# Kernel optimization log

Measured on AMD Instinct MI355X. Metric: run time of the kernel, lower is better.

The kernel has to match this reference:

```python
import jax, jax.numpy as jnp
import numpy as np

H = W = 128
R = 2
H2, W2 = H // R, W // R
TOPK = 3
NSEG = H * W + 1  # segment 0 = background


def _ccl(binary):
    """8-connected component labeling via iterative max-label propagation.
    binary: [H,W] bool. Returns int32 labels, 0 = background; each component
    gets a unique (arbitrary) positive id = max pixel index in the component."""
    idx = jnp.arange(1, H * W + 1, dtype=jnp.int32).reshape(H, W)
    lab0 = jnp.where(binary, idx, 0)

    def cond(c):
        return c[1]

    def body(c):
        lab, _ = c
        nb = jax.lax.reduce_window(lab, jnp.int32(0), jax.lax.max,
                                   (3, 3), (1, 1), 'SAME')  # 3x3 incl. self
        new = jnp.where(binary, nb, 0)
        return new, jnp.any(new != lab)

    lab, _ = jax.lax.while_loop(cond, body, (lab0, jnp.bool_(True)))
    return lab


def _process_one(prob_i, feat_i):
    """prob_i: [1,H,W], feat_i: [Cf,H,W] -> [3*Cf, H2, W2]."""
    p = prob_i[0]
    binary = p > 0.5
    lab = _ccl(binary).reshape(-1)  # [H*W] segment ids

    ones = jnp.ones((H * W,), jnp.float32)
    count = jax.ops.segment_sum(ones, lab, num_segments=NSEG)
    conf_sum = jax.ops.segment_sum(p.reshape(-1), lab, num_segments=NSEG)
    mean_conf = conf_sum / jnp.maximum(count, 1.0)

    rows = jnp.repeat(jnp.arange(H, dtype=jnp.int32), W)
    cols = jnp.tile(jnp.arange(W, dtype=jnp.int32), H)
    min_r = jax.ops.segment_min(rows, lab, num_segments=NSEG)
    max_r = jax.ops.segment_max(rows, lab, num_segments=NSEG)
    min_c = jax.ops.segment_min(cols, lab, num_segments=NSEG)
    max_c = jax.ops.segment_max(cols, lab, num_segments=NSEG)

    valid = (count > 0) & (jnp.arange(NSEG) > 0)
    score = jnp.where(valid, mean_conf, -jnp.inf)
    _, top_idx = jax.lax.top_k(score, TOPK)  # regions sorted by mean confidence
    K = jnp.sum(valid.astype(jnp.int32))     # number of connected regions

    # duplication rules: K==0 -> full image x3; K==1 -> [f0,f0,f0];
    # K==2 -> [f0,f0,f1]; K>=3 -> [f0,f1,f2]
    i0, i1 = top_idx[0], top_idx[1]
    slots = jnp.where(K >= 3, top_idx,
            jnp.where(K == 2, jnp.stack([i0, i0, i1]),
                      jnp.stack([i0, i0, i0])))

    mr = jnp.where(K > 0, min_r[slots], 0)
    Mr = jnp.where(K > 0, max_r[slots] + 1, H)  # bbox half-open, regionprops style
    mc = jnp.where(K > 0, min_c[slots], 0)
    Mc = jnp.where(K > 0, max_c[slots] + 1, W)

    def crop(a, b, c, d):
        # PyTorch nearest interpolate: src = floor(dst * in/out)
        r = a + (jnp.arange(H2) * (b - a)) // H2
        cc = c + (jnp.arange(W2) * (d - c)) // W2
        return feat_i[:, r][:, :, cc]  # [Cf, H2, W2]

    out = jax.vmap(crop)(mr, Mr, mc, Mc)  # [3, Cf, H2, W2]
    return out.reshape(-1, H2, W2)         # [3*Cf, H2, W2]


def setup_inputs() -> dict:
    key = jax.random.key(0)
    k1, k2 = jax.random.split(key)
    prob = jax.random.uniform(k1, (16, 1, H, W), dtype=jnp.float32)
    feat = jax.random.normal(k2, (16, 192, H, W), dtype=jnp.float32)
    return {"prob": prob, "feat": feat}


def reference(prob, feat):
    return jax.vmap(_process_one)(prob, feat)  # [B, 3*Cf, H2, W2]
```

## Files before the change

### kernel.cpp

```cpp
#include <hip/hip_runtime.h>
#include <limits.h>

#define HH 128
#define WW_ 128
#define HW 16384
#define NB 16
#define CF 192
#define H2 64
#define W2 64
#define NRUN 8192
#define NCOMP 4096

typedef float vf4 __attribute__((ext_vector_type(4)));
typedef unsigned long long ull;


__device__ inline int uf_find(int* par, int x) {
    volatile int* vp = (volatile int*)par;
    int p = vp[x];
    while (p != x) {
        int g = vp[p];
        vp[x] = g;
        x = g;
        p = vp[x];
    }
    return x;
}

__device__ inline void uf_union(int* par, int a, int b) {
    int ra = uf_find(par, a);
    int rb = uf_find(par, b);
    while (ra != rb) {
        if (ra < rb) { int t = ra; ra = rb; rb = t; }
        int old = atomicCAS(&par[ra], ra, rb);
        if (old == ra) return;
        ra = uf_find(par, old);
        rb = uf_find(par, rb);
    }
}


__device__ inline int getbit2(ull lo, ull hi, int c) {
    return (int)(((c < 64) ? (lo >> c) : (hi >> (c - 64))) & 1ULL);
}

__device__ inline int leading_ones(ull v) {
    ull nv = ~v;
    return (nv == 0ULL) ? 64 : __clzll(nv);
}

__device__ inline int trailing_ones(ull v) {
    ull nv = ~v;
    return (nv == 0ULL) ? 64 : (__ffsll(nv) - 1);
}

__device__ inline int run_start_col(ull lo, ull hi, int c) {
    if (c < 64) {
        int ones = leading_ones(lo << (63 - c));
        return c - ones + 1;
    }
    int ones = leading_ones(hi << (127 - c));
    int rs = c - ones + 1;
    if (rs == 64) rs -= leading_ones(lo);
    return rs;
}

__device__ inline int run_end_col(ull lo, ull hi, int c) {
    if (c >= 64) {
        return c + trailing_ones(hi >> (c - 64)) - 1;
    }
    int e = c + trailing_ones(lo >> c) - 1;
    if (e == 63) e += trailing_ones(hi);
    return e;
}

__device__ inline int run_index(ull rs_lo, ull rs_hi, int cs) {
    if (cs < 64)  return __popcll(rs_lo & ((1ULL << cs) - 1ULL));
    if (cs == 64) return __popcll(rs_lo);
    return __popcll(rs_lo) + __popcll(rs_hi & ((1ULL << (cs - 64)) - 1ULL));
}

__device__ inline void top3_ins(float s, int id, int x,
    float& s0, float& s1, float& s2,
    int& i0, int& i1, int& i2,
    int& x0, int& x1, int& x2)
{
    if (x < 0) return;
    if (s > s0 || (s == s0 && id < i0)) {
        s2 = s1; i2 = i1; x2 = x1;
        s1 = s0; i1 = i0; x1 = x0;
        s0 = s;  i0 = id; x0 = x;
    } else if (s > s1 || (s == s1 && id < i1)) {
        s2 = s1; i2 = i1; x2 = x1;
        s1 = s;  i1 = id; x1 = x;
    } else if (s > s2 || (s == s2 && id < i2)) {
        s2 = s;  i2 = id; x2 = x;
    }
}


__global__ __launch_bounds__(1024) void ccl_kernel(
    const float* __restrict__ prob, int* __restrict__ bbox)
{
    __shared__ int parent[NRUN];
    __shared__ ull rowmask[HH][2];
    __shared__ ull rsmask[HH][2];
    __shared__ int nrunrow[HH];
    __shared__ int   lcnt[NCOMP];
    __shared__ float lconf[NCOMP];
    __shared__ int lminr[NCOMP], lmaxr[NCOMP];
    __shared__ int lminc[NCOMP], lmaxc[NCOMP];
    __shared__ int lmaxid[NCOMP];
    __shared__ int snroots;
    __shared__ float wss[48];
    __shared__ int wid_[48], wrx[48];

    const int b = blockIdx.x;
    const int tid = threadIdx.x;
    const float* p = prob + (size_t)b * HW;

    if (tid == 0) snroots = 0;

    #pragma unroll
    for (int k = 0; k < HW / 1024; ++k) {
        int i = k * 1024 + tid;
        ull m = __ballot(p[i] > 0.5f);
        if ((tid & 63) == 0) rowmask[i >> 7][(i >> 6) & 1] = m;
    }
    for (int j = tid; j < NCOMP; j += 1024) {
        lcnt[j] = 0; lconf[j] = 0.f;
        lminr[j] = INT_MAX; lmaxr[j] = -1;
        lminc[j] = INT_MAX; lmaxc[j] = -1;
        lmaxid[j] = 0;
    }
    __syncthreads();

    for (int r = tid; r < HH; r += 1024) {
        ull lo = rowmask[r][0], hi = rowmask[r][1];
        ull rs_lo = lo & ~(lo << 1);
        ull rs_hi = hi & ~((hi << 1) | (lo >> 63));
        rsmask[r][0] = rs_lo; rsmask[r][1] = rs_hi;
        nrunrow[r] = __popcll(rs_lo) + __popcll(rs_hi);
    }
    __syncthreads();

    for (int rid = tid; rid < NRUN; rid += 1024)
        if ((rid & 63) < nrunrow[rid >> 6]) parent[rid] = rid;
    __syncthreads();

    for (int s = 1; s <= 64; s <<= 1) {
        const int items = (64 / s) * WW_;
        for (int it = tid; it < items; it += 1024) {
            int k = it >> 7, c = it & 127;
            int r = s * (2 * k + 1);
            ull lo = rowmask[r][0], hi = rowmask[r][1];
            if (!getbit2(lo, hi, c)) continue;
            ull ulo = rowmask[r - 1][0], uhi = rowmask[r - 1][1];
            int l  = (c > 0)   ? getbit2(lo, hi, c - 1) : 0;
            int rt = (c < 127) ? getbit2(lo, hi, c + 1) : 0;
            int up = getbit2(ulo, uhi, c);
            int ul = (c > 0)   ? getbit2(ulo, uhi, c - 1) : 0;
            int ur = (c < 127) ? getbit2(ulo, uhi, c + 1) : 0;
            bool u1 = up && !(l && ul);
            bool u2 = !up && ul && !l;
            bool u3 = !up && ur && !rt;
            if (!(u1 | u2 | u3)) continue;
            ull rs_lo = rsmask[r][0], rs_hi = rsmask[r][1];
            ull urs_lo = rsmask[r - 1][0], urs_hi = rsmask[r - 1][1];
            int rid = (r << 6) + run_index(rs_lo, rs_hi, run_start_col(lo, hi, c));
            int ub = (r - 1) << 6;
            if (u1) uf_union(parent, rid, ub + run_index(urs_lo, urs_hi, run_start_col(ulo, uhi, c)));
            if (u2) uf_union(parent, rid, ub + run_index(urs_lo, urs_hi, run_start_col(ulo, uhi, c - 1)));
            if (u3) uf_union(parent, rid, ub + run_index(urs_lo, urs_hi, run_start_col(ulo, uhi, c + 1)));
        }
        __syncthreads();
        for (int rid = tid; rid < NRUN; rid += 1024)
            if ((rid & 63) < nrunrow[rid >> 6]) parent[rid] = uf_find(parent, rid);
        __syncthreads();
    }

    for (int rid = tid; rid < NRUN; rid += 1024) {
        if ((rid & 63) < nrunrow[rid >> 6] && parent[rid] == rid) {
            int idx = atomicAdd(&snroots, 1);
            parent[rid] = NRUN + idx;
        }
    }
    __syncthreads();

    {
        int row = tid >> 3;
        int w0 = (tid & 7) * 16;
        ull lo = rowmask[row][0], hi = rowmask[row][1];
        ull rs_lo = rsmask[row][0], rs_hi = rsmask[row][1];
        ull seg = ((w0 < 64) ? (rs_lo >> w0) : (rs_hi >> (w0 - 64))) & 0xFFFFULL;
        int curIdx = -1, aCnt = 0, aMinc = 0, aMaxc = 0, aMaxid = 0;
        float aConf = 0.f;
        while (seg) {
            int c = w0 + (__ffsll(seg) - 1);
            seg &= seg - 1;
            int e = run_end_col(lo, hi, c);
            int rid = (row << 6) + run_index(rs_lo, rs_hi, c);
            int v = parent[rid];
            int idx = (v >= NRUN) ? (v - NRUN) : (parent[v] - NRUN);
            float s = 0.f;
            for (int j = c; j <= e; ++j) s += p[(row << 7) + j];
            if (idx == curIdx) {
                aCnt += e - c + 1; aConf += s;
                aMaxc = e; aMaxid = (row << 7) + e + 1;
            } else {
                if (curIdx >= 0) {
                    atomicAdd(&lcnt[curIdx], aCnt);
                    atomicAdd(&lconf[curIdx], aConf);
                    atomicMin(&lminr[curIdx], row);
                    atomicMax(&lmaxr[curIdx], row);
                    atomicMin(&lminc[curIdx], aMinc);
                    atomicMax(&lmaxc[curIdx], aMaxc);
                    atomicMax(&lmaxid[curIdx], aMaxid);
                }
                curIdx = idx; aCnt = e - c + 1; aConf = s;
                aMinc = c; aMaxc = e; aMaxid = (row << 7) + e + 1;
            }
        }
        if (curIdx >= 0) {
            atomicAdd(&lcnt[curIdx], aCnt);
            atomicAdd(&lconf[curIdx], aConf);
            atomicMin(&lminr[curIdx], row);
            atomicMax(&lmaxr[curIdx], row);
            atomicMin(&lminc[curIdx], aMinc);
            atomicMax(&lmaxc[curIdx], aMaxc);
            atomicMax(&lmaxid[curIdx], aMaxid);
        }
    }
    __syncthreads();

    const int n = snroots;
    float s0 = -INFINITY, s1 = -INFINITY, s2 = -INFINITY;
    int i0 = INT_MAX, i1 = INT_MAX, i2 = INT_MAX;
    int x0 = -1, x1 = -1, x2 = -1;
    for (int j = tid; j < n; j += 1024) {
        float s = lconf[j] / (float)lcnt[j];
        top3_ins(s, lmaxid[j], j, s0, s1, s2, i0, i1, i2, x0, x1, x2);
    }
    for (int off = 32; off; off >>= 1) {
        float bs0 = __shfl_xor(s0, off), bs1 = __shfl_xor(s1, off), bs2 = __shfl_xor(s2, off);
        int bi0 = __shfl_xor(i0, off), bi1 = __shfl_xor(i1, off), bi2 = __shfl_xor(i2, off);
        int bx0 = __shfl_xor(x0, off), bx1 = __shfl_xor(x1, off), bx2 = __shfl_xor(x2, off);
        top3_ins(bs0, bi0, bx0, s0, s1, s2, i0, i1, i2, x0, x1, x2);
        top3_ins(bs1, bi1, bx1, s0, s1, s2, i0, i1, i2, x0, x1, x2);
        top3_ins(bs2, bi2, bx2, s0, s1, s2, i0, i1, i2, x0, x1, x2);
    }
    if ((tid & 63) == 0) {
        int w = tid >> 6;
        wss[w * 3 + 0] = s0; wid_[w * 3 + 0] = i0; wrx[w * 3 + 0] = x0;
        wss[w * 3 + 1] = s1; wid_[w * 3 + 1] = i1; wrx[w * 3 + 1] = x1;
        wss[w * 3 + 2] = s2; wid_[w * 3 + 2] = i2; wrx[w * 3 + 2] = x2;
    }
    __syncthreads();

    if (tid == 0) {
        float t0 = -INFINITY, t1 = -INFINITY, t2 = -INFINITY;
        int ti0 = INT_MAX, ti1 = INT_MAX, ti2 = INT_MAX;
        int tx0 = -1, tx1 = -1, tx2 = -1;
        for (int t = 0; t < 48; ++t)
            top3_ins(wss[t], wid_[t], wrx[t], t0, t1, t2, ti0, ti1, ti2, tx0, tx1, tx2);
        int K = n;
        int roots[3];
        if (K >= 3)      { roots[0] = tx0; roots[1] = tx1; roots[2] = tx2; }
        else if (K == 2) { roots[0] = tx0; roots[1] = tx0; roots[2] = tx1; }
        else             { roots[0] = tx0; roots[1] = tx0; roots[2] = tx0; }
        for (int slot = 0; slot < 3; ++slot) {
            int mr, h, mc, w;
            if (K == 0) { mr = 0; h = HH; mc = 0; w = WW_; }
            else {
                int rt = roots[slot];
                mr = lminr[rt]; h = lmaxr[rt] + 1 - mr;
                mc = lminc[rt]; w = lmaxc[rt] + 1 - mc;
            }
            int* o = bbox + (b * 3 + slot) * 4;
            o[0] = mr; o[1] = h; o[2] = mc; o[3] = w;
        }
    }
}


__global__ __launch_bounds__(256) void crop_kernel(
    const float* __restrict__ feat, const int* __restrict__ bbox,
    float* __restrict__ out)
{
    const int gid = blockIdx.x * 256 + threadIdx.x;
    const int x4 = gid & 15;
    const int y  = (gid >> 4) & 63;
    const int t  = gid >> 10;
    const int c  = t % CF;
    const int bs = t / CF;
    const int* bb = bbox + bs * 4;
    const int mr = bb[0], h = bb[1], mc = bb[2], w = bb[3];
    const int r = mr + ((y * h) >> 6);
    const int bimg = bs / 3;
    const float* row = feat + (((size_t)bimg * CF + c) * HH + r) * WW_;
    const int x = x4 * 4;
    vf4 v;
    v.x = row[mc + (((x + 0) * w) >> 6)];
    v.y = row[mc + (((x + 1) * w) >> 6)];
    v.z = row[mc + (((x + 2) * w) >> 6)];
    v.w = row[mc + (((x + 3) * w) >> 6)];
    __builtin_nontemporal_store(v, (vf4*)out + gid);
}


extern "C" void kernel_launch(void* const* d_in, const int* in_sizes, int n_in,
                              void* d_out, int out_size, void* d_ws, size_t ws_size,
                              hipStream_t stream) {
    const float* prob = (const float*)d_in[0];
    const float* feat = (const float*)d_in[1];
    float* out = (float*)d_out;

    int* bbox = (int*)d_ws;

    hipLaunchKernelGGL(ccl_kernel, dim3(NB), dim3(1024), 0, stream,
                       prob, bbox);
    const int total4 = NB * 3 * CF * H2 * (W2 / 4);
    hipLaunchKernelGGL(crop_kernel, dim3(total4 / 256), dim3(256), 0, stream,
                       feat, bbox, out);
}
```

Before: 399.9 us.

## Single-pass union-find CCL, stage probabilities in LDS, bbox only for winners

Drops the hierarchical log-step merge schedule, which ran 7 rounds of unions each followed by a full path-compression pass, and replaces it with one pass of concurrent unions over all rows and then a single compression. Probability values are cached in shared memory so per-run confidence sums no longer reread global memory. Root numbering uses a wave ballot with one atomic per wave instead of one atomic per root. Bounding boxes are computed in a second scan only for the three winning components, which removes four per-component atomic arrays and the run-merging logic. In exchange, run-level atomics now fire per run instead of per merged segment, and heavy concurrent unions may contend more.

```diff
diff --git a/kernel.cpp b/kernel.cpp
--- a/kernel.cpp
+++ b/kernel.cpp
@@ -103,17 +103,18 @@
     const float* __restrict__ prob, int* __restrict__ bbox)
 {
     __shared__ int parent[NRUN];
+    __shared__ float pbuf[HW];
     __shared__ ull rowmask[HH][2];
     __shared__ ull rsmask[HH][2];
     __shared__ int nrunrow[HH];
     __shared__ int   lcnt[NCOMP];
     __shared__ float lconf[NCOMP];
-    __shared__ int lminr[NCOMP], lmaxr[NCOMP];
-    __shared__ int lminc[NCOMP], lmaxc[NCOMP];
     __shared__ int lmaxid[NCOMP];
     __shared__ int snroots;
     __shared__ float wss[48];
     __shared__ int wid_[48], wrx[48];
+    __shared__ int winner[3];
+    __shared__ int w_minr[3], w_maxr[3], w_minc[3], w_maxc[3];
 
     const int b = blockIdx.x;
     const int tid = threadIdx.x;
@@ -124,14 +125,15 @@
     #pragma unroll
     for (int k = 0; k < HW / 1024; ++k) {
         int i = k * 1024 + tid;
-        ull m = __ballot(p[i] > 0.5f);
+        float v = p[i];
+        pbuf[i] = v;
+        ull m = __ballot(v > 0.5f);
         if ((tid & 63) == 0) rowmask[i >> 7][(i >> 6) & 1] = m;
     }
+    #pragma unroll
+    for (int k = 0; k < NRUN / 1024; ++k) parent[k * 1024 + tid] = k * 1024 + tid;
     for (int j = tid; j < NCOMP; j += 1024) {
-        lcnt[j] = 0; lconf[j] = 0.f;
-        lminr[j] = INT_MAX; lmaxr[j] = -1;
-        lminc[j] = INT_MAX; lmaxc[j] = -1;
-        lmaxid[j] = 0;
+        lcnt[j] = 0; lconf[j] = 0.f; lmaxid[j] = 0;
     }
     __syncthreads();
 
@@ -144,46 +146,46 @@
     }
     __syncthreads();
 
+    for (int k = 0; k < HW / 1024; ++k) {
+        int i = k * 1024 + tid;
+        int r = i >> 7, c = i & 127;
+        if (r == 0) continue;
+        ull lo = rowmask[r][0], hi = rowmask[r][1];
+        if (!getbit2(lo, hi, c)) continue;
+        ull ulo = rowmask[r - 1][0], uhi = rowmask[r - 1][1];
+        int l  = (c > 0)   ? getbit2(lo, hi, c - 1) : 0;
+        int rt = (c < 127) ? getbit2(lo, hi, c + 1) : 0;
+        int up = getbit2(ulo, uhi, c);
+        int ul = (c > 0)   ? getbit2(ulo, uhi, c - 1) : 0;
+        int ur = (c < 127) ? getbit2(ulo, uhi, c + 1) : 0;
+        bool u1 = up && !(l && ul);
+        bool u2 = !up && ul && !l;
+        bool u3 = !up && ur && !rt;
+        if (!(u1 | u2 | u3)) continue;
+        ull rs_lo = rsmask[r][0], rs_hi = rsmask[r][1];
+        ull urs_lo = rsmask[r - 1][0], urs_hi = rsmask[r - 1][1];
+        int rid = (r << 6) + run_index(rs_lo, rs_hi, run_start_col(lo, hi, c));
+        int ub = (r - 1) << 6;
+        if (u1) uf_union(parent, rid, ub + run_index(urs_lo, urs_hi, run_start_col(ulo, uhi, c)));
+        if (u2) uf_union(parent, rid, ub + run_index(urs_lo, urs_hi, run_start_col(ulo, uhi, c - 1)));
+        if (u3) uf_union(parent, rid, ub + run_index(urs_lo, urs_hi, run_start_col(ulo, uhi, c + 1)));
+    }
+    __syncthreads();
+
     for (int rid = tid; rid < NRUN; rid += 1024)
-        if ((rid & 63) < nrunrow[rid >> 6]) parent[rid] = rid;
-    __syncthreads();
-
-    for (int s = 1; s <= 64; s <<= 1) {
-        const int items = (64 / s) * WW_;
-        for (int it = tid; it < items; it += 1024) {
-            int k = it >> 7, c = it & 127;
-            int r = s * (2 * k + 1);
-            ull lo = rowmask[r][0], hi = rowmask[r][1];
-            if (!getbit2(lo, hi, c)) continue;
-            ull ulo = rowmask[r - 1][0], uhi = rowmask[r - 1][1];
-            int l  = (c > 0)   ? getbit2(lo, hi, c - 1) : 0;
-            int rt = (c < 127) ? getbit2(lo, hi, c + 1) : 0;
-            int up = getbit2(ulo, uhi, c);
-            int ul = (c > 0)   ? getbit2(ulo, uhi, c - 1) : 0;
-            int ur = (c < 127) ? getbit2(ulo, uhi, c + 1) : 0;
-            bool u1 = up && !(l && ul);
-            bool u2 = !up && ul && !l;
-            bool u3 = !up && ur && !rt;
-            if (!(u1 | u2 | u3)) continue;
-            ull rs_lo = rsmask[r][0], rs_hi = rsmask[r][1];
-            ull urs_lo = rsmask[r - 1][0], urs_hi = rsmask[r - 1][1];
-            int rid = (r << 6) + run_index(rs_lo, rs_hi, run_start_col(lo, hi, c));
-            int ub = (r - 1) << 6;
-            if (u1) uf_union(parent, rid, ub + run_index(urs_lo, urs_hi, run_start_col(ulo, uhi, c)));
-            if (u2) uf_union(parent, rid, ub + run_index(urs_lo, urs_hi, run_start_col(ulo, uhi, c - 1)));
-            if (u3) uf_union(parent, rid, ub + run_index(urs_lo, urs_hi, run_start_col(ulo, uhi, c + 1)));
-        }
-        __syncthreads();
-        for (int rid = tid; rid < NRUN; rid += 1024)
-            if ((rid & 63) < nrunrow[rid >> 6]) parent[rid] = uf_find(parent, rid);
-        __syncthreads();
-    }
+        if ((rid & 63) < nrunrow[rid >> 6]) parent[rid] = uf_find(parent, rid);
+    __syncthreads();
 
     for (int rid = tid; rid < NRUN; rid += 1024) {
-        if ((rid & 63) < nrunrow[rid >> 6] && parent[rid] == rid) {
-            int idx = atomicAdd(&snroots, 1);
-            parent[rid] = NRUN + idx;
-        }
+        bool isroot = ((rid & 63) < nrunrow[rid >> 6]) && parent[rid] == rid;
+        ull m = __ballot(isroot);
+        int lane = tid & 63;
+        int cntw = __popcll(m);
+        int baseIdx = 0;
+        if (lane == 0 && cntw) baseIdx = atomicAdd(&snroots, cntw);
+        baseIdx = __shfl(baseIdx, 0);
+        if (isroot)
+            parent[rid] = NRUN + baseIdx + __popcll(m & ((1ULL << lane) - 1ULL));
     }
     __syncthreads();
 
@@ -193,8 +195,6 @@
         ull lo = rowmask[row][0], hi = rowmask[row][1];
         ull rs_lo = rsmask[row][0], rs_hi = rsmask[row][1];
         ull seg = ((w0 < 64) ? (rs_lo >> w0) : (rs_hi >> (w0 - 64))) & 0xFFFFULL;
-        int curIdx = -1, aCnt = 0, aMinc = 0, aMaxc = 0, aMaxid = 0;
-        float aConf = 0.f;
         while (seg) {
             int c = w0 + (__ffsll(seg) - 1);
             seg &= seg - 1;
@@ -203,57 +203,42 @@
             int v = parent[rid];
             int idx = (v >= NRUN) ? (v - NRUN) : (parent[v] - NRUN);
             float s = 0.f;
-            for (int j = c; j <= e; ++j) s += p[(row << 7) + j];
-            if (idx == curIdx) {
-                aCnt += e - c + 1; aConf += s;
-                aMaxc = e; aMaxid = (row << 7) + e + 1;
-            } else {
-                if (curIdx >= 0) {
-                    atomicAdd(&lcnt[curIdx], aCnt);
-                    atomicAdd(&lconf[curIdx], aConf);
-                    atomicMin(&lminr[curIdx], row);
-                    atomicMax(&lmaxr[curIdx], row);
-                    atomicMin(&lminc[curIdx], aMinc);
-                    atomicMax(&lmaxc[curIdx], aMaxc);
-                    atomicMax(&lmaxid[curIdx], aMaxid);
-                }
-                curIdx = idx; aCnt = e - c + 1; aConf = s;
-                aMinc = c; aMaxc = e; aMaxid = (row << 7) + e + 1;
-            }
-        }
-        if (curIdx >= 0) {
-            atomicAdd(&lcnt[curIdx], aCnt);
-            atomicAdd(&lconf[curIdx], aConf);
-            atomicMin(&lminr[curIdx], row);
-            atomicMax(&lmaxr[curIdx], row);
-            atomicMin(&lminc[curIdx], aMinc);
-            atomicMax(&lmaxc[curIdx], aMaxc);
-            atomicMax(&lmaxid[curIdx], aMaxid);
+            for (int j = c; j <= e; ++j) s += pbuf[(row << 7) + j];
+            atomicAdd(&lcnt[idx], e - c + 1);
+            atomicAdd(&lconf[idx], s);
+            atomicMax(&lmaxid[idx], (row << 7) + e + 1);
         }
     }
     __syncthreads();
 
     const int n = snroots;
-    float s0 = -INFINITY, s1 = -INFINITY, s2 = -INFINITY;
-    int i0 = INT_MAX, i1 = INT_MAX, i2 = INT_MAX;
-    int x0 = -1, x1 = -1, x2 = -1;
-    for (int j = tid; j < n; j += 1024) {
-        float s = lconf[j] / (float)lcnt[j];
-        top3_ins(s, lmaxid[j], j, s0, s1, s2, i0, i1, i2, x0, x1, x2);
-    }
-    for (int off = 32; off; off >>= 1) {
-        float bs0 = __shfl_xor(s0, off), bs1 = __shfl_xor(s1, off), bs2 = __shfl_xor(s2, off);
-        int bi0 = __shfl_xor(i0, off), bi1 = __shfl_xor(i1, off), bi2 = __shfl_xor(i2, off);
-        int bx0 = __shfl_xor(x0, off), bx1 = __shfl_xor(x1, off), bx2 = __shfl_xor(x2, off);
-        top3_ins(bs0, bi0, bx0, s0, s1, s2, i0, i1, i2, x0, x1, x2);
-        top3_ins(bs1, bi1, bx1, s0, s1, s2, i0, i1, i2, x0, x1, x2);
-        top3_ins(bs2, bi2, bx2, s0, s1, s2, i0, i1, i2, x0, x1, x2);
-    }
-    if ((tid & 63) == 0) {
-        int w = tid >> 6;
-        wss[w * 3 + 0] = s0; wid_[w * 3 + 0] = i0; wrx[w * 3 + 0] = x0;
-        wss[w * 3 + 1] = s1; wid_[w * 3 + 1] = i1; wrx[w * 3 + 1] = x1;
-        wss[w * 3 + 2] = s2; wid_[w * 3 + 2] = i2; wrx[w * 3 + 2] = x2;
+    {
+        float s0 = -INFINITY, s1 = -INFINITY, s2 = -INFINITY;
+        int i0 = INT_MAX, i1 = INT_MAX, i2 = INT_MAX;
+        int x0 = -1, x1 = -1, x2 = -1;
+        for (int j = tid; j < n; j += 1024) {
+            float s = lconf[j] / (float)lcnt[j];
+            top3_ins(s, lmaxid[j], j, s0, s1, s2, i0, i1, i2, x0, x1, x2);
+        }
+        for (int off = 32; off; off >>= 1) {
+            float bs0 = __shfl_xor(s0, off), bs1 = __shfl_xor(s1, off), bs2 = __shfl_xor(s2, off);
+            int bi0 = __shfl_xor(i0, off), bi1 = __shfl_xor(i1, off), bi2 = __shfl_xor(i2, off);
+            int bx0 = __shfl_xor(x0, off), bx1 = __shfl_xor(x1, off), bx2 = __shfl_xor(x2, off);
+            top3_ins(bs0, bi0, bx0, s0, s1, s2, i0, i1, i2, x0, x1, x2);
+            top3_ins(bs1, bi1, bx1, s0, s1, s2, i0, i1, i2, x0, x1, x2);
+            top3_ins(bs2, bi2, bx2, s0, s1, s2, i0, i1, i2, x0, x1, x2);
+        }
+        if ((tid & 63) == 0) {
+            int w = tid >> 6;
+            wss[w * 3 + 0] = s0; wid_[w * 3 + 0] = i0; wrx[w * 3 + 0] = x0;
+            wss[w * 3 + 1] = s1; wid_[w * 3 + 1] = i1; wrx[w * 3 + 1] = x1;
+            wss[w * 3 + 2] = s2; wid_[w * 3 + 2] = i2; wrx[w * 3 + 2] = x2;
+        }
+        if (tid >= 64 && tid < 67) {
+            int s = tid - 64;
+            w_minr[s] = INT_MAX; w_maxr[s] = -1;
+            w_minc[s] = INT_MAX; w_maxc[s] = -1;
+        }
     }
     __syncthreads();
 
@@ -264,21 +249,52 @@
         for (int t = 0; t < 48; ++t)
             top3_ins(wss[t], wid_[t], wrx[t], t0, t1, t2, ti0, ti1, ti2, tx0, tx1, tx2);
         int K = n;
-        int roots[3];
-        if (K >= 3)      { roots[0] = tx0; roots[1] = tx1; roots[2] = tx2; }
-        else if (K == 2) { roots[0] = tx0; roots[1] = tx0; roots[2] = tx1; }
-        else             { roots[0] = tx0; roots[1] = tx0; roots[2] = tx0; }
-        for (int slot = 0; slot < 3; ++slot) {
-            int mr, h, mc, w;
-            if (K == 0) { mr = 0; h = HH; mc = 0; w = WW_; }
-            else {
-                int rt = roots[slot];
-                mr = lminr[rt]; h = lmaxr[rt] + 1 - mr;
-                mc = lminc[rt]; w = lmaxc[rt] + 1 - mc;
+        if (K >= 3)      { winner[0] = tx0; winner[1] = tx1; winner[2] = tx2; }
+        else if (K == 2) { winner[0] = tx0; winner[1] = tx0; winner[2] = tx1; }
+        else if (K == 1) { winner[0] = tx0; winner[1] = tx0; winner[2] = tx0; }
+        else             { winner[0] = -1;  winner[1] = -1;  winner[2] = -1;  }
+    }
+    __syncthreads();
+
+    {
+        int row = tid >> 3;
+        int w0 = (tid & 7) * 16;
+        ull lo = rowmask[row][0], hi = rowmask[row][1];
+        ull rs_lo = rsmask[row][0], rs_hi = rsmask[row][1];
+        ull seg = ((w0 < 64) ? (rs_lo >> w0) : (rs_hi >> (w0 - 64))) & 0xFFFFULL;
+        int wn0 = winner[0], wn1 = winner[1], wn2 = winner[2];
+        while (seg) {
+            int c = w0 + (__ffsll(seg) - 1);
+            seg &= seg - 1;
+            int rid = (row << 6) + run_index(rs_lo, rs_hi, c);
+            int v = parent[rid];
+            int idx = (v >= NRUN) ? (v - NRUN) : (parent[v] - NRUN);
+            if (idx != wn0 && idx != wn1 && idx != wn2) continue;
+            int e = run_end_col(lo, hi, c);
+            #pragma unroll
+            for (int s = 0; s < 3; ++s) {
+                int wn = (s == 0) ? wn0 : (s == 1) ? wn1 : wn2;
+                if (idx == wn) {
+                    atomicMin(&w_minr[s], row);
+                    atomicMax(&w_maxr[s], row);
+                    atomicMin(&w_minc[s], c);
+                    atomicMax(&w_maxc[s], e);
+                }
             }
-            int* o = bbox + (b * 3 + slot) * 4;
-            o[0] = mr; o[1] = h; o[2] = mc; o[3] = w;
-        }
+        }
+    }
+    __syncthreads();
+
+    if (tid < 3) {
+        int s = tid;
+        int mr, h, mc, w;
+        if (winner[s] < 0) { mr = 0; h = HH; mc = 0; w = WW_; }
+        else {
+            mr = w_minr[s]; h = w_maxr[s] + 1 - mr;
+            mc = w_minc[s]; w = w_maxc[s] + 1 - mc;
+        }
+        int* o = bbox + (b * 3 + s) * 4;
+        o[0] = mr; o[1] = h; o[2] = mc; o[3] = w;
     }
 }
 
```

Result: faster. 387.2 us, median of 2 (-3.2%).

## Replace log-step CCL merge with single-pass run-overlap union-find

Applied to the files above, without the earlier changes.

Replaces the hierarchical multi-level union pass, which needed a flatten step and two barriers per level, with a single pass. In that pass every run is unioned with each overlapping run in the row above, and the ballot, row-mask and run-mask setup is fused into one phase. Root numbering now uses wave ballots with one atomic per wave, and the flattening pointer chase is folded into that same loop. Per-run stats are accumulated with direct atomics instead of being merged in registers first, and only the live component entries are initialized. The crop kernel now emits two float4 per thread on half the grid. The aim is to cut barrier and pass count in the serial single-block-per-image CCL stage, at the cost of more shared-memory atomic contention.

```diff
diff --git a/kernel.cpp b/kernel.cpp
--- a/kernel.cpp
+++ b/kernel.cpp
@@ -39,6 +39,13 @@
     }
 }
 
+__device__ inline int walk_term(int* par, int x) {
+    volatile int* vp = (volatile int*)par;
+    int p = vp[x];
+    while (p < NRUN && p != x) { x = p; p = vp[x]; }
+    return (p >= NRUN) ? p : x;
+}
+
 
 __device__ inline int getbit2(ull lo, ull hi, int c) {
     return (int)(((c < 64) ? (lo >> c) : (hi >> (c - 64))) & 1ULL);
@@ -78,6 +85,17 @@
     if (cs < 64)  return __popcll(rs_lo & ((1ULL << cs) - 1ULL));
     if (cs == 64) return __popcll(rs_lo);
     return __popcll(rs_lo) + __popcll(rs_hi & ((1ULL << (cs - 64)) - 1ULL));
+}
+
+__device__ inline void span_mask(int a, int b, ull& mlo, ull& mhi) {
+    ull one = ~0ULL;
+    int bl = (b < 63) ? b : 63;
+    mlo = (a <= 63) ? (((bl == 63) ? one : ((1ULL << (bl + 1)) - 1)) & ~((1ULL << a) - 1)) : 0ULL;
+    if (b >= 64) {
+        int a2 = (a >= 64) ? a - 64 : 0;
+        int b2 = b - 64;
+        mhi = ((b2 == 63) ? one : ((1ULL << (b2 + 1)) - 1)) & ~((1ULL << a2) - 1);
+    } else mhi = 0ULL;
 }
 
 __device__ inline void top3_ins(float s, int id, int x,
@@ -117,73 +135,95 @@
 
     const int b = blockIdx.x;
     const int tid = threadIdx.x;
+    const int lane = tid & 63;
     const float* p = prob + (size_t)b * HW;
 
     if (tid == 0) snroots = 0;
 
-    #pragma unroll
-    for (int k = 0; k < HW / 1024; ++k) {
-        int i = k * 1024 + tid;
-        ull m = __ballot(p[i] > 0.5f);
-        if ((tid & 63) == 0) rowmask[i >> 7][(i >> 6) & 1] = m;
-    }
-    for (int j = tid; j < NCOMP; j += 1024) {
+    {
+        int wv = tid >> 6;
+        #pragma unroll
+        for (int k = 0; k < 8; ++k) {
+            int row = wv * 8 + k;
+            const float* rp = p + (row << 7);
+            ull m0 = __ballot(rp[lane] > 0.5f);
+            ull m1 = __ballot(rp[64 + lane] > 0.5f);
+            if (lane == 0) {
+                rowmask[row][0] = m0; rowmask[row][1] = m1;
+                ull rs_lo = m0 & ~(m0 << 1);
+                ull rs_hi = m1 & ~((m1 << 1) | (m0 >> 63));
+                rsmask[row][0] = rs_lo; rsmask[row][1] = rs_hi;
+                nrunrow[row] = __popcll(rs_lo) + __popcll(rs_hi);
+            }
+        }
+        #pragma unroll
+        for (int k = 0; k < NRUN / 1024; ++k)
+            parent[k * 1024 + tid] = k * 1024 + tid;
+    }
+    __syncthreads();
+
+    {
+        int row = tid >> 3;
+        int w0 = (tid & 7) * 16;
+        if (row > 0) {
+            ull lo = rowmask[row][0], hi = rowmask[row][1];
+            ull rs_lo = rsmask[row][0], rs_hi = rsmask[row][1];
+            ull seg = ((w0 < 64) ? (rs_lo >> w0) : (rs_hi >> (w0 - 64))) & 0xFFFFULL;
+            if (seg) {
+                ull ulo = rowmask[row - 1][0], uhi = rowmask[row - 1][1];
+                ull urs_lo = rsmask[row - 1][0], urs_hi = rsmask[row - 1][1];
+                int ub = (row - 1) << 6;
+                while (seg) {
+                    int c = w0 + (__ffsll(seg) - 1);
+                    seg &= seg - 1;
+                    int e = run_end_col(lo, hi, c);
+                    int rid = (row << 6) + run_index(rs_lo, rs_hi, c);
+                    int s0 = (c > 0) ? c - 1 : 0;
+                    int s1 = (e < 127) ? e + 1 : 127;
+                    if (getbit2(ulo, uhi, s0))
+                        uf_union(parent, rid,
+                                 ub + run_index(urs_lo, urs_hi, run_start_col(ulo, uhi, s0)));
+                    if (s1 > s0) {
+                        ull mlo, mhi;
+                        span_mask(s0 + 1, s1, mlo, mhi);
+                        ull h_lo = urs_lo & mlo, h_hi = urs_hi & mhi;
+                        while (h_lo) {
+                            int cs = __ffsll(h_lo) - 1; h_lo &= h_lo - 1;
+                            uf_union(parent, rid, ub + run_index(urs_lo, urs_hi, cs));
+                        }
+                        while (h_hi) {
+                            int cs = 64 + __ffsll(h_hi) - 1; h_hi &= h_hi - 1;
+                            uf_union(parent, rid, ub + run_index(urs_lo, urs_hi, cs));
+                        }
+                    }
+                }
+            }
+        }
+    }
+    __syncthreads();
+
+    for (int rid = tid; rid < NRUN; rid += 1024) {
+        bool valid = (rid & 63) < nrunrow[rid >> 6];
+        bool isroot = valid && parent[rid] == rid;
+        ull m = __ballot(isroot);
+        if (m) {
+            int baseIdx = 0;
+            if (lane == 0) baseIdx = atomicAdd(&snroots, __popcll(m));
+            baseIdx = __shfl(baseIdx, 0);
+            if (isroot)
+                parent[rid] = NRUN + baseIdx + __popcll(m & ((1ULL << lane) - 1ULL));
+        }
+        if (valid && !isroot)
+            parent[rid] = walk_term(parent, rid);
+    }
+    __syncthreads();
+
+    const int n = snroots;
+    for (int j = tid; j < n; j += 1024) {
         lcnt[j] = 0; lconf[j] = 0.f;
         lminr[j] = INT_MAX; lmaxr[j] = -1;
         lminc[j] = INT_MAX; lmaxc[j] = -1;
         lmaxid[j] = 0;
-    }
-    __syncthreads();
-
-    for (int r = tid; r < HH; r += 1024) {
-        ull lo = rowmask[r][0], hi = rowmask[r][1];
-        ull rs_lo = lo & ~(lo << 1);
-        ull rs_hi = hi & ~((hi << 1) | (lo >> 63));
-        rsmask[r][0] = rs_lo; rsmask[r][1] = rs_hi;
-        nrunrow[r] = __popcll(rs_lo) + __popcll(rs_hi);
-    }
-    __syncthreads();
-
-    for (int rid = tid; rid < NRUN; rid += 1024)
-        if ((rid & 63) < nrunrow[rid >> 6]) parent[rid] = rid;
-    __syncthreads();
-
-    for (int s = 1; s <= 64; s <<= 1) {
-        const int items = (64 / s) * WW_;
-        for (int it = tid; it < items; it += 1024) {
-            int k = it >> 7, c = it & 127;
-            int r = s * (2 * k + 1);
-            ull lo = rowmask[r][0], hi = rowmask[r][1];
-            if (!getbit2(lo, hi, c)) continue;
-            ull ulo = rowmask[r - 1][0], uhi = rowmask[r - 1][1];
-            int l  = (c > 0)   ? getbit2(lo, hi, c - 1) : 0;
-            int rt = (c < 127) ? getbit2(lo, hi, c + 1) : 0;
-            int up = getbit2(ulo, uhi, c);
-            int ul = (c > 0)   ? getbit2(ulo, uhi, c - 1) : 0;
-            int ur = (c < 127) ? getbit2(ulo, uhi, c + 1) : 0;
-            bool u1 = up && !(l && ul);
-            bool u2 = !up && ul && !l;
-            bool u3 = !up && ur && !rt;
-            if (!(u1 | u2 | u3)) continue;
-            ull rs_lo = rsmask[r][0], rs_hi = rsmask[r][1];
-            ull urs_lo = rsmask[r - 1][0], urs_hi = rsmask[r - 1][1];
-            int rid = (r << 6) + run_index(rs_lo, rs_hi, run_start_col(lo, hi, c));
-            int ub = (r - 1) << 6;
-            if (u1) uf_union(parent, rid, ub + run_index(urs_lo, urs_hi, run_start_col(ulo, uhi, c)));
-            if (u2) uf_union(parent, rid, ub + run_index(urs_lo, urs_hi, run_start_col(ulo, uhi, c - 1)));
-            if (u3) uf_union(parent, rid, ub + run_index(urs_lo, urs_hi, run_start_col(ulo, uhi, c + 1)));
-        }
-        __syncthreads();
-        for (int rid = tid; rid < NRUN; rid += 1024)
-            if ((rid & 63) < nrunrow[rid >> 6]) parent[rid] = uf_find(parent, rid);
-        __syncthreads();
-    }
-
-    for (int rid = tid; rid < NRUN; rid += 1024) {
-        if ((rid & 63) < nrunrow[rid >> 6] && parent[rid] == rid) {
-            int idx = atomicAdd(&snroots, 1);
-            parent[rid] = NRUN + idx;
-        }
     }
     __syncthreads();
 
@@ -193,8 +233,6 @@
         ull lo = rowmask[row][0], hi = rowmask[row][1];
         ull rs_lo = rsmask[row][0], rs_hi = rsmask[row][1];
         ull seg = ((w0 < 64) ? (rs_lo >> w0) : (rs_hi >> (w0 - 64))) & 0xFFFFULL;
-        int curIdx = -1, aCnt = 0, aMinc = 0, aMaxc = 0, aMaxid = 0;
-        float aConf = 0.f;
         while (seg) {
             int c = w0 + (__ffsll(seg) - 1);
             seg &= seg - 1;
@@ -204,56 +242,39 @@
             int idx = (v >= NRUN) ? (v - NRUN) : (parent[v] - NRUN);
             float s = 0.f;
             for (int j = c; j <= e; ++j) s += p[(row << 7) + j];
-            if (idx == curIdx) {
-                aCnt += e - c + 1; aConf += s;
-                aMaxc = e; aMaxid = (row << 7) + e + 1;
-            } else {
-                if (curIdx >= 0) {
-                    atomicAdd(&lcnt[curIdx], aCnt);
-                    atomicAdd(&lconf[curIdx], aConf);
-                    atomicMin(&lminr[curIdx], row);
-                    atomicMax(&lmaxr[curIdx], row);
-                    atomicMin(&lminc[curIdx], aMinc);
-                    atomicMax(&lmaxc[curIdx], aMaxc);
-                    atomicMax(&lmaxid[curIdx], aMaxid);
-                }
-                curIdx = idx; aCnt = e - c + 1; aConf = s;
-                aMinc = c; aMaxc = e; aMaxid = (row << 7) + e + 1;
-            }
-        }
-        if (curIdx >= 0) {
-            atomicAdd(&lcnt[curIdx], aCnt);
-            atomicAdd(&lconf[curIdx], aConf);
-            atomicMin(&lminr[curIdx], row);
-            atomicMax(&lmaxr[curIdx], row);
-            atomicMin(&lminc[curIdx], aMinc);
-            atomicMax(&lmaxc[curIdx], aMaxc);
-            atomicMax(&lmaxid[curIdx], aMaxid);
-        }
-    }
-    __syncthreads();
-
-    const int n = snroots;
-    float s0 = -INFINITY, s1 = -INFINITY, s2 = -INFINITY;
-    int i0 = INT_MAX, i1 = INT_MAX, i2 = INT_MAX;
-    int x0 = -1, x1 = -1, x2 = -1;
-    for (int j = tid; j < n; j += 1024) {
-        float s = lconf[j] / (float)lcnt[j];
-        top3_ins(s, lmaxid[j], j, s0, s1, s2, i0, i1, i2, x0, x1, x2);
-    }
-    for (int off = 32; off; off >>= 1) {
-        float bs0 = __shfl_xor(s0, off), bs1 = __shfl_xor(s1, off), bs2 = __shfl_xor(s2, off);
-        int bi0 = __shfl_xor(i0, off), bi1 = __shfl_xor(i1, off), bi2 = __shfl_xor(i2, off);
-        int bx0 = __shfl_xor(x0, off), bx1 = __shfl_xor(x1, off), bx2 = __shfl_xor(x2, off);
-        top3_ins(bs0, bi0, bx0, s0, s1, s2, i0, i1, i2, x0, x1, x2);
-        top3_ins(bs1, bi1, bx1, s0, s1, s2, i0, i1, i2, x0, x1, x2);
-        top3_ins(bs2, bi2, bx2, s0, s1, s2, i0, i1, i2, x0, x1, x2);
-    }
-    if ((tid & 63) == 0) {
-        int w = tid >> 6;
-        wss[w * 3 + 0] = s0; wid_[w * 3 + 0] = i0; wrx[w * 3 + 0] = x0;
-        wss[w * 3 + 1] = s1; wid_[w * 3 + 1] = i1; wrx[w * 3 + 1] = x1;
-        wss[w * 3 + 2] = s2; wid_[w * 3 + 2] = i2; wrx[w * 3 + 2] = x2;
+            atomicAdd(&lcnt[idx], e - c + 1);
+            atomicAdd(&lconf[idx], s);
+            atomicMin(&lminr[idx], row);
+            atomicMax(&lmaxr[idx], row);
+            atomicMin(&lminc[idx], c);
+            atomicMax(&lmaxc[idx], e);
+            atomicMax(&lmaxid[idx], (row << 7) + e + 1);
+        }
+    }
+    __syncthreads();
+
+    {
+        float s0 = -INFINITY, s1 = -INFINITY, s2 = -INFINITY;
+        int i0 = INT_MAX, i1 = INT_MAX, i2 = INT_MAX;
+        int x0 = -1, x1 = -1, x2 = -1;
+        for (int j = tid; j < n; j += 1024) {
+            float s = lconf[j] / (float)lcnt[j];
+            top3_ins(s, lmaxid[j], j, s0, s1, s2, i0, i1, i2, x0, x1, x2);
+        }
+        for (int off = 32; off; off >>= 1) {
+            float bs0 = __shfl_xor(s0, off), bs1 = __shfl_xor(s1, off), bs2 = __shfl_xor(s2, off);
+            int bi0 = __shfl_xor(i0, off), bi1 = __shfl_xor(i1, off), bi2 = __shfl_xor(i2, off);
+            int bx0 = __shfl_xor(x0, off), bx1 = __shfl_xor(x1, off), bx2 = __shfl_xor(x2, off);
+            top3_ins(bs0, bi0, bx0, s0, s1, s2, i0, i1, i2, x0, x1, x2);
+            top3_ins(bs1, bi1, bx1, s0, s1, s2, i0, i1, i2, x0, x1, x2);
+            top3_ins(bs2, bi2, bx2, s0, s1, s2, i0, i1, i2, x0, x1, x2);
+        }
+        if (lane == 0) {
+            int w = tid >> 6;
+            wss[w * 3 + 0] = s0; wid_[w * 3 + 0] = i0; wrx[w * 3 + 0] = x0;
+            wss[w * 3 + 1] = s1; wid_[w * 3 + 1] = i1; wrx[w * 3 + 1] = x1;
+            wss[w * 3 + 2] = s2; wid_[w * 3 + 2] = i2; wrx[w * 3 + 2] = x2;
+        }
     }
     __syncthreads();
 
@@ -288,9 +309,10 @@
     float* __restrict__ out)
 {
     const int gid = blockIdx.x * 256 + threadIdx.x;
-    const int x4 = gid & 15;
-    const int y  = (gid >> 4) & 63;
-    const int t  = gid >> 10;
+    const int o4 = gid * 2;
+    const int x4 = o4 & 15;
+    const int y  = (o4 >> 4) & 63;
+    const int t  = o4 >> 10;
     const int c  = t % CF;
     const int bs = t / CF;
     const int* bb = bbox + bs * 4;
@@ -299,12 +321,17 @@
     const int bimg = bs / 3;
     const float* row = feat + (((size_t)bimg * CF + c) * HH + r) * WW_;
     const int x = x4 * 4;
-    vf4 v;
-    v.x = row[mc + (((x + 0) * w) >> 6)];
-    v.y = row[mc + (((x + 1) * w) >> 6)];
-    v.z = row[mc + (((x + 2) * w) >> 6)];
-    v.w = row[mc + (((x + 3) * w) >> 6)];
-    __builtin_nontemporal_store(v, (vf4*)out + gid);
+    vf4 v0, v1;
+    v0.x = row[mc + (((x + 0) * w) >> 6)];
+    v0.y = row[mc + (((x + 1) * w) >> 6)];
+    v0.z = row[mc + (((x + 2) * w) >> 6)];
+    v0.w = row[mc + (((x + 3) * w) >> 6)];
+    v1.x = row[mc + (((x + 4) * w) >> 6)];
+    v1.y = row[mc + (((x + 5) * w) >> 6)];
+    v1.z = row[mc + (((x + 6) * w) >> 6)];
+    v1.w = row[mc + (((x + 7) * w) >> 6)];
+    __builtin_nontemporal_store(v0, (vf4*)out + o4);
+    __builtin_nontemporal_store(v1, (vf4*)out + o4 + 1);
 }
 
 
@@ -320,6 +347,6 @@
     hipLaunchKernelGGL(ccl_kernel, dim3(NB), dim3(1024), 0, stream,
                        prob, bbox);
     const int total4 = NB * 3 * CF * H2 * (W2 / 4);
-    hipLaunchKernelGGL(crop_kernel, dim3(total4 / 256), dim3(256), 0, stream,
+    hipLaunchKernelGGL(crop_kernel, dim3(total4 / 512), dim3(256), 0, stream,
                        feat, bbox, out);
 }
```

After: 392.6 us. Within noise of the previous version (-1.8%).
